# Optimization experiments

Hardware: AMD Instinct MI355X
Metric: run time of the kernel (lower is better)

Reference implementation:

```python
import jax, jax.numpy as jnp
import numpy as np

D_IN, E, K = 128, 256, 16
LN_EPS = 1e-5


def _layernorm(h, g, b):
    mu = jnp.mean(h, axis=-1, keepdims=True)
    var = jnp.mean(jnp.square(h - mu), axis=-1, keepdims=True)
    return (h - mu) * jax.lax.rsqrt(var + LN_EPS) * g + b


def _gelu(h):
    return jax.nn.gelu(h, approximate=False)  # torch F.gelu default = exact erf


def setup_inputs() -> dict:
    key = jax.random.key(0)
    ks = jax.random.split(key, 8)
    B, N = 8, 2048
    def lin(k, fan_in, fan_out):
        bound = 1.0 / np.sqrt(fan_in)
        return jax.random.uniform(k, (fan_in, fan_out), jnp.float32, -bound, bound)
    return {
        "x": jax.random.normal(ks[0], (B, N, D_IN), jnp.float32),
        "coordinates": jax.random.normal(ks[1], (B, N, 3), jnp.float32),
        "W1": lin(ks[2], 2 * D_IN, E), "b1": jnp.zeros((E,), jnp.float32),
        "g1": jnp.ones((E,), jnp.float32), "be1": jnp.zeros((E,), jnp.float32),
        "W2": lin(ks[3], E, E), "b2": jnp.zeros((E,), jnp.float32),
        "g2": jnp.ones((E,), jnp.float32), "be2": jnp.zeros((E,), jnp.float32),
        "W3": lin(ks[4], E, E), "b3": jnp.zeros((E,), jnp.float32),
        "g3": jnp.ones((E,), jnp.float32), "be3": jnp.zeros((E,), jnp.float32),
        "Ws": lin(ks[5], D_IN, E), "bs": jnp.zeros((E,), jnp.float32),
    }


def reference(x, coordinates, W1, b1, g1, be1, W2, b2, g2, be2, W3, b3, g3, be3, Ws, bs):
    B, N, D = x.shape
    # --- dynamic kNN graph: squared euclidean distances (sqrt is monotone, skip it) ---
    sq = jnp.sum(coordinates * coordinates, axis=-1)                 # [B,N]
    d2 = sq[:, :, None] + sq[:, None, :] - 2.0 * jnp.einsum(
        'bnc,bmc->bnm', coordinates, coordinates)                    # [B,N,N]
    d2 = jnp.maximum(d2, 0.0)
    _, idx = jax.lax.top_k(-d2, K)                                   # [B,N,K] nearest (incl. self)
    # --- gather neighbor features: neighbors[b,n,j] = x[b, idx[b,n,j]] ---
    neighbors = jax.vmap(lambda xb, ib: xb[ib])(x, idx)              # [B,N,K,D]
    central = jnp.broadcast_to(x[:, :, None, :], (B, N, K, D))       # [B,N,K,D]
    edge = jnp.concatenate([central, neighbors - central], axis=-1)  # [B,N,K,2D]
    # --- edge MLP: (Linear -> LN -> GELU) x3 ---
    h = _gelu(_layernorm(edge @ W1 + b1, g1, be1))
    h = _gelu(_layernorm(h @ W2 + b2, g2, be2))
    h = _gelu(_layernorm(h @ W3 + b3, g3, be3))                      # [B,N,K,E]
    # --- max aggregate over neighbors + shortcut ---
    agg = jnp.max(h, axis=2)                                         # [B,N,E]
    return _gelu(agg + x @ Ws + bs)
```

## Files before the change

### kernel.cpp

```cpp
#include <hip/hip_runtime.h>
#include <hip/hip_bf16.h>
#include <math.h>

#define B_ 8
#define N_ 2048
#define D_ 128
#define E_ 256
#define K_ 16
#define LN_EPS 1e-5f

typedef short bf16x8 __attribute__((ext_vector_type(8)));
typedef float f32x4 __attribute__((ext_vector_type(4)));
typedef float f32x2 __attribute__((ext_vector_type(2)));

__device__ __forceinline__ float sq3_ref(float x, float y, float z) {
#pragma clang fp contract(off)
    float s = x * x + y * y;
    s = s + z * z;
    return s;
}
__device__ __forceinline__ float d2_ref(float qx, float qy, float qz, float sqq,
                                        float mx, float my, float mz, float sqm) {
#pragma clang fp contract(off)
    float dot = mx * qx + my * qy;
    dot = dot + mz * qz;
    float t1 = sqq + sqm;
    float t2 = 2.0f * dot;
    float d2 = t1 - t2;
    return d2 > 0.0f ? d2 : 0.0f;
}

__device__ __forceinline__ unsigned pack2(float a, float b) {
    union { __hip_bfloat162 h2; unsigned u; } cv;
    cv.h2 = __float22bfloat162_rn(float2{a, b});
    return cv.u;
}

__device__ __forceinline__ f32x2 gelu2(f32x2 v) {
    const f32x2 w = v * v;
    f32x2 inner = w * 0.044715f;
    inner.x += 1.0f; inner.y += 1.0f;
    const f32x2 ue = (v * -2.3022083f) * inner;
    f32x2 t;
    t.x = __builtin_amdgcn_exp2f(ue.x);
    t.y = __builtin_amdgcn_exp2f(ue.y);
    f32x2 den = t;
    den.x += 1.0f; den.y += 1.0f;
    f32x2 r;
    r.x = __builtin_amdgcn_rcpf(den.x);
    r.y = __builtin_amdgcn_rcpf(den.y);
    return v * r;
}

__device__ __forceinline__ float dpp_rowmax16(float v) {
    int x = __float_as_int(v);
    v = fmaxf(v, __int_as_float(__builtin_amdgcn_mov_dpp(x, 0xB1, 0xF, 0xF, true)));
    x = __float_as_int(v);
    v = fmaxf(v, __int_as_float(__builtin_amdgcn_mov_dpp(x, 0x4E, 0xF, 0xF, true)));
    x = __float_as_int(v);
    v = fmaxf(v, __int_as_float(__builtin_amdgcn_mov_dpp(x, 0x141, 0xF, 0xF, true)));
    x = __float_as_int(v);
    v = fmaxf(v, __int_as_float(__builtin_amdgcn_mov_dpp(x, 0x140, 0xF, 0xF, true)));
    return v;
}

__global__ __launch_bounds__(512) void prep_kernel(
    const float* __restrict__ coords, const float* __restrict__ x,
    const float* __restrict__ W1, const float* __restrict__ W2,
    const float* __restrict__ W3, const float* __restrict__ Ws,
    const float* __restrict__ bs,
    int* __restrict__ knn_out, short* __restrict__ WF, float* __restrict__ out)
{
    __shared__ float smem[4 * N_ + 8];
    const int bid = blockIdx.x;
    const int tid = threadIdx.x;

    if (bid < 2048) {
        float (*lc)[N_] = (float(*)[N_])smem;
        float* lsq = smem + 3 * N_;
        int* cnt = (int*)(smem + 4 * N_);
        const int wave = tid >> 6;
        const int lane = tid & 63;
        const int p = bid * 8 + wave;
        const int b = p >> 11;
        const int n0 = p & (N_ - 1);
        const float* cb = coords + (size_t)b * N_ * 3;
        for (int i = tid; i < N_ * 3; i += 512) {
            int n = i / 3, c = i - 3 * n;
            lc[c][n] = cb[i];
        }
        __syncthreads();
        for (int n = tid; n < N_; n += 512) lsq[n] = sq3_ref(lc[0][n], lc[1][n], lc[2][n]);
        __syncthreads();

        const float qx = lc[0][n0], qy = lc[1][n0], qz = lc[2][n0], sqq = lsq[n0];
        unsigned key[32];
#pragma unroll
        for (int j = 0; j < 32; ++j) {
            const int m = j * 64 + lane;
            key[j] = __float_as_uint(d2_ref(qx, qy, qz, sqq, lc[0][m], lc[1][m], lc[2][m], lsq[m]));
        }

        unsigned prefix = 0;
        int rem = K_, setc = N_, bshift = 0;
        bool bounded = false;
        for (int bit = 31; bit >= 0; --bit) {
            const unsigned want = prefix << 1;
            int c = 0;
#pragma unroll
            for (int j = 0; j < 32; ++j) c += ((key[j] >> bit) == want) ? 1 : 0;
            for (int off = 1; off < 64; off <<= 1) c += __shfl_xor(c, off, 64);
            if (rem <= c) { prefix = want; setc = c; }
            else          { prefix = want | 1u; rem -= c; setc -= c; }
            bshift = bit;
            if (setc == rem) { bounded = true; break; }
        }

        if (lane == 0) cnt[wave] = 0;
        int* op = knn_out + (size_t)p * K_;
        const unsigned long long BE = bounded ? (((unsigned long long)prefix + 1ull) << bshift)
                                              : (unsigned long long)prefix;
#pragma unroll
        for (int j = 0; j < 32; ++j) {
            if ((unsigned long long)key[j] < BE) {
                int s = atomicAdd(&cnt[wave], 1);
                op[s] = j * 64 + lane;
            }
        }
        if (!bounded) {
            const unsigned V = prefix;
#pragma unroll
            for (int j = 0; j < 32; ++j) {
                if (rem > 0) {
                    unsigned long long mask = __ballot(key[j] == V);
                    int below = __popcll(mask & ((1ull << lane) - 1ull));
                    if (key[j] == V && below < rem) {
                        int s = atomicAdd(&cnt[wave], 1);
                        op[s] = j * 64 + lane;
                    }
                    rem -= __popcll(mask);
                }
            }
        }
    } else if (bid < 2096) {
        const int unit = (bid - 2048) * 8 + (tid >> 6);
        const int lane = tid & 63;
        const int g = lane >> 4, e = lane & 15;
        const int L = unit >> 7;
        const int t = unit & 127;
        const int kt = t >> 4, mt = t & 15;
        const float* W = (L == 0) ? W1 : (L == 1) ? W2 : W3;
        const int f = 16 * mt + e;
        unsigned v[4];
#pragma unroll
        for (int i2 = 0; i2 < 4; ++i2) {
            const int k = 32 * kt + 8 * g + 2 * i2;
            v[i2] = pack2(W[(size_t)k * E_ + f], W[(size_t)(k + 1) * E_ + f]);
        }
        uint4 u; u.x = v[0]; u.y = v[1]; u.z = v[2]; u.w = v[3];
        *reinterpret_cast<uint4*>(WF + ((size_t)unit * 64 + lane) * 8) = u;
    } else {
        const int wave = tid >> 6;
        const int lane = tid & 63;
        const int e = lane & 15;
        const int g = lane >> 4;
        const int p0 = ((bid - 2096) * 8 + wave) * 16;
        const float* xr = x + (size_t)(p0 + e) * D_;

        f32x4 acc[16];
        const f32x4 z4 = {0.f, 0.f, 0.f, 0.f};
#pragma unroll
        for (int mt = 0; mt < 16; ++mt) acc[mt] = z4;

#pragma unroll
        for (int kt = 0; kt < 4; ++kt) {
            const float4 xa = *(const float4*)(xr + kt * 32 + g * 8);
            const float4 xb = *(const float4*)(xr + kt * 32 + g * 8 + 4);
            union { unsigned u[4]; bf16x8 v; } bx;
            bx.u[0] = pack2(xa.x, xa.y); bx.u[1] = pack2(xa.z, xa.w);
            bx.u[2] = pack2(xb.x, xb.y); bx.u[3] = pack2(xb.z, xb.w);
            const float* Wsrc = Ws + (size_t)(32 * kt + 8 * g) * E_ + e;
#pragma unroll
            for (int mt = 0; mt < 16; ++mt) {
                const float* wp = Wsrc + 16 * mt;
                float w[8];
#pragma unroll
                for (int i = 0; i < 8; ++i) w[i] = wp[(size_t)i * E_];
                union { unsigned u[4]; bf16x8 v; } a;
                a.u[0] = pack2(w[0], w[1]); a.u[1] = pack2(w[2], w[3]);
                a.u[2] = pack2(w[4], w[5]); a.u[3] = pack2(w[6], w[7]);
                acc[mt] = __builtin_amdgcn_mfma_f32_16x16x32_bf16(a.v, bx.v, acc[mt], 0, 0, 0);
            }
        }
#pragma unroll
        for (int mt = 0; mt < 16; ++mt) {
            const float4 bsv = *(const float4*)(bs + 16 * mt + 4 * g);
            float4 o;
            o.x = acc[mt][0] + bsv.x; o.y = acc[mt][1] + bsv.y;
            o.z = acc[mt][2] + bsv.z; o.w = acc[mt][3] + bsv.w;
            *(float4*)(out + (size_t)(p0 + e) * E_ + 16 * mt + 4 * g) = o;
        }
    }
}

#define WCHUNKS 24

__device__ __forceinline__ void stage_chunk(const short* __restrict__ WF,
                                            short* __restrict__ dst,
                                            int c, int wave, int lane) {
    const short* src = WF + ((size_t)(c << 4) << 9);
#pragma unroll
    for (int i = 0; i < 4; ++i) {
        const int slot = (i << 8) + (wave << 6);
        const short* gp = src + ((size_t)(slot + lane) << 3);
        short* lp = dst + ((size_t)slot << 3);
        __builtin_amdgcn_global_load_lds(
            (const __attribute__((address_space(1))) void*)gp,
            (__attribute__((address_space(3))) void*)lp, 16, 0, 0);
    }
}

__global__ __launch_bounds__(256, 3) void edgeconv_mfma(
    const float* __restrict__ x, const int* __restrict__ knn,
    const short* __restrict__ WF,
    const float* __restrict__ b1, const float* __restrict__ g1, const float* __restrict__ be1,
    const float* __restrict__ b2, const float* __restrict__ g2, const float* __restrict__ be2,
    const float* __restrict__ b3, const float* __restrict__ g3, const float* __restrict__ be3,
    float* __restrict__ out)
{
    __shared__ short Hl[2][2][4096];
    __shared__ short Wbuf[8192];
    __shared__ float4 Xch[2][2][16];
    __shared__ float Pl[768];
    const int tid  = threadIdx.x;
    const int wave = tid >> 6;
    const int lane = tid & 63;
    const int wq = wave & 1;
    const int pr = wave >> 1;
    const int e = lane & 15;
    const int g = lane >> 4;
    const int p = blockIdx.x * 4 + wave;
    const int b = p >> 11;
    const int n = p & (N_ - 1);
    const unsigned swz = (unsigned)((e & 7) << 4);
    char* Hown = (char*)&Hl[pr][wq][0];
    char* Hp0  = (char*)&Hl[pr][0][0];
    char* Hp1  = (char*)&Hl[pr][1][0];

    {
        const float4* xr = (const float4*)(x + ((size_t)b * N_ + n) * D_);
        const int nb = knn[(size_t)p * K_ + e];
        const float4* nr = (const float4*)(x + ((size_t)b * N_ + nb) * D_);
#pragma unroll
        for (int c2 = 0; c2 < 8; ++c2) {
            const float4 cv = xr[8 * g + c2];
            const float4 nv = nr[8 * g + c2];
            const int base = (e << 9) + (g << 6) + (c2 << 3);
            *(uint2*)(Hown + (base ^ swz)) = make_uint2(pack2(cv.x, cv.y), pack2(cv.z, cv.w));
            *(uint2*)(Hown + ((base + 256) ^ swz)) =
                make_uint2(pack2(nv.x - cv.x, nv.y - cv.y), pack2(nv.z - cv.z, nv.w - cv.w));
        }
    }

    f32x4 acc0[8], acc1[8];
    const f32x4 z4 = {0.f, 0.f, 0.f, 0.f};

    for (int L = 0; L < 3; ++L) {
        const float* bL  = (L == 0) ? b1  : (L == 1) ? b2  : b3;
        const float* gL  = (L == 0) ? g1  : (L == 1) ? g2  : g3;
        const float* beL = (L == 0) ? be1 : (L == 1) ? be2 : be3;
#pragma unroll
        for (int mtl = 0; mtl < 8; ++mtl) { acc0[mtl] = z4; acc1[mtl] = z4; }

        for (int kt = 0; kt < 8; ++kt) {
            const int c = L * 8 + kt;
            __syncthreads();
            const int offB = (int)((unsigned)((e << 9) + (kt << 6) + (g << 4)) ^ swz);
            const bf16x8 Bc0 = *(const bf16x8*)(Hp0 + offB);
            const bf16x8 Bc1 = *(const bf16x8*)(Hp1 + offB);
            stage_chunk(WF, Wbuf, c, wave, lane);
            asm volatile("s_waitcnt vmcnt(0)" ::: "memory");
            __syncthreads();
            if (kt == 0) {
                Pl[tid]       = bL[tid];
                Pl[256 + tid] = gL[tid];
                Pl[512 + tid] = beL[tid];
            }
            __builtin_amdgcn_s_setprio(1);
#pragma unroll
            for (int mtl = 0; mtl < 8; ++mtl) {
                const bf16x8 a = *(const bf16x8*)(Wbuf + ((((wq << 3) + mtl) << 6) + lane) * 8);
                acc0[mtl] = __builtin_amdgcn_mfma_f32_16x16x32_bf16(a, Bc0, acc0[mtl], 0, 0, 0);
                acc1[mtl] = __builtin_amdgcn_mfma_f32_16x16x32_bf16(a, Bc1, acc1[mtl], 0, 0, 0);
            }
            __builtin_amdgcn_s_setprio(0);
        }

        f32x2 s2_0 = {0.f, 0.f}, q2_0 = {0.f, 0.f};
        f32x2 s2_1 = {0.f, 0.f}, q2_1 = {0.f, 0.f};
#pragma unroll
        for (int mtl = 0; mtl < 8; ++mtl) {
            const int mtg = (wq << 3) + mtl;
            const float4 bv = *(const float4*)(Pl + mtg * 16 + (g << 2));
            const f32x2 blo = {bv.x, bv.y}, bhi = {bv.z, bv.w};
            f32x2 a0lo = {acc0[mtl][0], acc0[mtl][1]};
            f32x2 a0hi = {acc0[mtl][2], acc0[mtl][3]};
            f32x2 a1lo = {acc1[mtl][0], acc1[mtl][1]};
            f32x2 a1hi = {acc1[mtl][2], acc1[mtl][3]};
            a0lo = a0lo + blo; a0hi = a0hi + bhi;
            a1lo = a1lo + blo; a1hi = a1hi + bhi;
            s2_0 = s2_0 + a0lo; s2_0 = s2_0 + a0hi;
            q2_0 = q2_0 + a0lo * a0lo; q2_0 = q2_0 + a0hi * a0hi;
            s2_1 = s2_1 + a1lo; s2_1 = s2_1 + a1hi;
            q2_1 = q2_1 + a1lo * a1lo; q2_1 = q2_1 + a1hi * a1hi;
            acc0[mtl][0] = a0lo.x; acc0[mtl][1] = a0lo.y;
            acc0[mtl][2] = a0hi.x; acc0[mtl][3] = a0hi.y;
            acc1[mtl][0] = a1lo.x; acc1[mtl][1] = a1lo.y;
            acc1[mtl][2] = a1hi.x; acc1[mtl][3] = a1hi.y;
        }
        float s0 = s2_0.x + s2_0.y, q0 = q2_0.x + q2_0.y;
        float s1 = s2_1.x + s2_1.y, q1 = q2_1.x + q2_1.y;
        s0 += __shfl_xor(s0, 16, 64); s0 += __shfl_xor(s0, 32, 64);
        q0 += __shfl_xor(q0, 16, 64); q0 += __shfl_xor(q0, 32, 64);
        s1 += __shfl_xor(s1, 16, 64); s1 += __shfl_xor(s1, 32, 64);
        q1 += __shfl_xor(q1, 16, 64); q1 += __shfl_xor(q1, 32, 64);
        if (lane < 16) Xch[pr][wq][e] = make_float4(s0, q0, s1, q1);
        __syncthreads();
        const float4 oX = Xch[pr][wq ^ 1][e];
        const float mu0 = (s0 + oX.x) * (1.0f / 256.0f);
        const float var0 = fmaf(-mu0, mu0, (q0 + oX.y) * (1.0f / 256.0f));
        const float rstd0 = rsqrtf(var0 + LN_EPS);
        const float mu1 = (s1 + oX.z) * (1.0f / 256.0f);
        const float var1 = fmaf(-mu1, mu1, (q1 + oX.w) * (1.0f / 256.0f));
        const float rstd1 = rsqrtf(var1 + LN_EPS);

#pragma unroll
        for (int mtl = 0; mtl < 8; ++mtl) {
            const int mtg = (wq << 3) + mtl;
            const float4 gv  = *(const float4*)(Pl + 256 + mtg * 16 + (g << 2));
            const float4 bev = *(const float4*)(Pl + 512 + mtg * 16 + (g << 2));
            const f32x2 glo = {gv.x, gv.y}, ghi = {gv.z, gv.w};
            const f32x2 belo = {bev.x, bev.y}, behi = {bev.z, bev.w};
            const f32x2 A0lo = glo * rstd0, A0hi = ghi * rstd0;
            const f32x2 C0lo = A0lo * (-mu0) + belo, C0hi = A0hi * (-mu0) + behi;
            const f32x2 v0lo = {acc0[mtl][0], acc0[mtl][1]};
            const f32x2 v0hi = {acc0[mtl][2], acc0[mtl][3]};
            const f32x2 r0lo = gelu2(v0lo * A0lo + C0lo);
            const f32x2 r0hi = gelu2(v0hi * A0hi + C0hi);
            const f32x2 A1lo = glo * rstd1, A1hi = ghi * rstd1;
            const f32x2 C1lo = A1lo * (-mu1) + belo, C1hi = A1hi * (-mu1) + behi;
            const f32x2 v1lo = {acc1[mtl][0], acc1[mtl][1]};
            const f32x2 v1hi = {acc1[mtl][2], acc1[mtl][3]};
            const f32x2 r1lo = gelu2(v1lo * A1lo + C1lo);
            const f32x2 r1hi = gelu2(v1hi * A1hi + C1hi);
            if (L < 2) {
                const int wb = (int)((unsigned)((e << 9) + (mtg << 5) + (g << 3)) ^ swz);
                *(uint2*)(Hp0 + wb) = make_uint2(pack2(r0lo.x, r0lo.y), pack2(r0hi.x, r0hi.y));
                *(uint2*)(Hp1 + wb) = make_uint2(pack2(r1lo.x, r1lo.y), pack2(r1hi.x, r1hi.y));
            } else {
                acc0[mtl][0] = r0lo.x; acc0[mtl][1] = r0lo.y;
                acc0[mtl][2] = r0hi.x; acc0[mtl][3] = r0hi.y;
                acc1[mtl][0] = r1lo.x; acc1[mtl][1] = r1lo.y;
                acc1[mtl][2] = r1hi.x; acc1[mtl][3] = r1hi.y;
            }
        }
    }

#pragma unroll
    for (int mtl = 0; mtl < 8; ++mtl) {
#pragma unroll
        for (int i = 0; i < 4; ++i) {
            acc0[mtl][i] = dpp_rowmax16(acc0[mtl][i]);
            acc1[mtl][i] = dpp_rowmax16(acc1[mtl][i]);
        }
    }
    float* Sb0 = (float*)Hp0;
    float* Sb1 = (float*)Hp1;
#pragma unroll
    for (int mtl = 0; mtl < 8; ++mtl) {
        if (e == mtl) {
            const int fo = (((wq << 3) + mtl) << 4) + (g << 2);
            *(float4*)(Sb0 + fo) = *(const float4*)&acc0[mtl];
            *(float4*)(Sb1 + fo) = *(const float4*)&acc1[mtl];
        }
    }
    __syncthreads();

    const int f0 = 16 * e + (g << 2);
    const float* SbO = wq ? Sb1 : Sb0;
    const float4 agg = *(const float4*)(SbO + f0);
    float* op = out + (size_t)p * E_ + f0;
    const float4 ssc = *(const float4*)op;
    f32x2 elo = {agg.x + ssc.x, agg.y + ssc.y};
    f32x2 ehi = {agg.z + ssc.z, agg.w + ssc.w};
    const f32x2 olo = gelu2(elo);
    const f32x2 ohi = gelu2(ehi);
    float4 o;
    o.x = olo.x; o.y = olo.y; o.z = ohi.x; o.w = ohi.y;
    *(float4*)op = o;
}

extern "C" void kernel_launch(void* const* d_in, const int* in_sizes, int n_in,
                              void* d_out, int out_size, void* d_ws, size_t ws_size,
                              hipStream_t stream) {
    const float* x      = (const float*)d_in[0];
    const float* coords = (const float*)d_in[1];
    const float* W1  = (const float*)d_in[2];
    const float* b1  = (const float*)d_in[3];
    const float* g1  = (const float*)d_in[4];
    const float* be1 = (const float*)d_in[5];
    const float* W2  = (const float*)d_in[6];
    const float* b2  = (const float*)d_in[7];
    const float* g2  = (const float*)d_in[8];
    const float* be2 = (const float*)d_in[9];
    const float* W3  = (const float*)d_in[10];
    const float* b3  = (const float*)d_in[11];
    const float* g3  = (const float*)d_in[12];
    const float* be3 = (const float*)d_in[13];
    const float* Ws  = (const float*)d_in[14];
    const float* bs  = (const float*)d_in[15];
    float* out = (float*)d_out;

    int*   knn = (int*)d_ws;
    short* WF  = (short*)((char*)d_ws + (1 << 20));

    prep_kernel<<<2048 + 48 + 128, 512, 0, stream>>>(
        coords, x, W1, W2, W3, Ws, bs, knn, WF, out);
    edgeconv_mfma<<<(B_ * N_) / 4, 256, 0, stream>>>(
        x, knn, WF, b1, g1, be1, b2, g2, be2, b3, g3, be3, out);
}
```

Before: 296.1 us.

## Read MFMA weight fragments directly from global, drop LDS staging and per-k-tile barriers

New measurement: 302.0 us. No clear change (+2.0%).

```diff
diff --git a/kernel.cpp b/kernel.cpp
--- a/kernel.cpp
+++ b/kernel.cpp
@@ -203,23 +203,6 @@
     }
 }
 
-#define WCHUNKS 24
-
-__device__ __forceinline__ void stage_chunk(const short* __restrict__ WF,
-                                            short* __restrict__ dst,
-                                            int c, int wave, int lane) {
-    const short* src = WF + ((size_t)(c << 4) << 9);
-#pragma unroll
-    for (int i = 0; i < 4; ++i) {
-        const int slot = (i << 8) + (wave << 6);
-        const short* gp = src + ((size_t)(slot + lane) << 3);
-        short* lp = dst + ((size_t)slot << 3);
-        __builtin_amdgcn_global_load_lds(
-            (const __attribute__((address_space(1))) void*)gp,
-            (__attribute__((address_space(3))) void*)lp, 16, 0, 0);
-    }
-}
-
 __global__ __launch_bounds__(256, 3) void edgeconv_mfma(
     const float* __restrict__ x, const int* __restrict__ knn,
     const short* __restrict__ WF,
@@ -229,9 +212,8 @@
     float* __restrict__ out)
 {
     __shared__ short Hl[2][2][4096];
-    __shared__ short Wbuf[8192];
     __shared__ float4 Xch[2][2][16];
-    __shared__ float Pl[768];
+    __shared__ float Pl[9 * 256];
     const int tid  = threadIdx.x;
     const int wave = tid >> 6;
     const int lane = tid & 63;
@@ -248,6 +230,12 @@
     char* Hp1  = (char*)&Hl[pr][1][0];
 
     {
+        const float* srcs[9] = {b1, g1, be1, b2, g2, be2, b3, g3, be3};
+#pragma unroll
+        for (int a = 0; a < 9; ++a) Pl[a * 256 + tid] = srcs[a][tid];
+    }
+
+    {
         const float4* xr = (const float4*)(x + ((size_t)b * N_ + n) * D_);
         const int nb = knn[(size_t)p * K_ + e];
         const float4* nr = (const float4*)(x + ((size_t)b * N_ + nb) * D_);
@@ -261,35 +249,27 @@
                 make_uint2(pack2(nv.x - cv.x, nv.y - cv.y), pack2(nv.z - cv.z, nv.w - cv.w));
         }
     }
+    __syncthreads();
 
     f32x4 acc0[8], acc1[8];
     const f32x4 z4 = {0.f, 0.f, 0.f, 0.f};
 
     for (int L = 0; L < 3; ++L) {
-        const float* bL  = (L == 0) ? b1  : (L == 1) ? b2  : b3;
-        const float* gL  = (L == 0) ? g1  : (L == 1) ? g2  : g3;
-        const float* beL = (L == 0) ? be1 : (L == 1) ? be2 : be3;
+        const float* PlL = &Pl[L * 768];
 #pragma unroll
         for (int mtl = 0; mtl < 8; ++mtl) { acc0[mtl] = z4; acc1[mtl] = z4; }
 
+        const short* AL = WF + (((size_t)(L * 128 + wq * 8)) << 9);
+
         for (int kt = 0; kt < 8; ++kt) {
-            const int c = L * 8 + kt;
-            __syncthreads();
             const int offB = (int)((unsigned)((e << 9) + (kt << 6) + (g << 4)) ^ swz);
             const bf16x8 Bc0 = *(const bf16x8*)(Hp0 + offB);
             const bf16x8 Bc1 = *(const bf16x8*)(Hp1 + offB);
-            stage_chunk(WF, Wbuf, c, wave, lane);
-            asm volatile("s_waitcnt vmcnt(0)" ::: "memory");
-            __syncthreads();
-            if (kt == 0) {
-                Pl[tid]       = bL[tid];
-                Pl[256 + tid] = gL[tid];
-                Pl[512 + tid] = beL[tid];
-            }
+            const short* Ak = AL + ((size_t)kt << 13);
             __builtin_amdgcn_s_setprio(1);
 #pragma unroll
             for (int mtl = 0; mtl < 8; ++mtl) {
-                const bf16x8 a = *(const bf16x8*)(Wbuf + ((((wq << 3) + mtl) << 6) + lane) * 8);
+                const bf16x8 a = *(const bf16x8*)(Ak + (mtl << 9) + (lane << 3));
                 acc0[mtl] = __builtin_amdgcn_mfma_f32_16x16x32_bf16(a, Bc0, acc0[mtl], 0, 0, 0);
                 acc1[mtl] = __builtin_amdgcn_mfma_f32_16x16x32_bf16(a, Bc1, acc1[mtl], 0, 0, 0);
             }
@@ -301,7 +281,7 @@
 #pragma unroll
         for (int mtl = 0; mtl < 8; ++mtl) {
             const int mtg = (wq << 3) + mtl;
-            const float4 bv = *(const float4*)(Pl + mtg * 16 + (g << 2));
+            const float4 bv = *(const float4*)(PlL + mtg * 16 + (g << 2));
             const f32x2 blo = {bv.x, bv.y}, bhi = {bv.z, bv.w};
             f32x2 a0lo = {acc0[mtl][0], acc0[mtl][1]};
             f32x2 a0hi = {acc0[mtl][2], acc0[mtl][3]};
@@ -337,8 +317,8 @@
 #pragma unroll
         for (int mtl = 0; mtl < 8; ++mtl) {
             const int mtg = (wq << 3) + mtl;
-            const float4 gv  = *(const float4*)(Pl + 256 + mtg * 16 + (g << 2));
-            const float4 bev = *(const float4*)(Pl + 512 + mtg * 16 + (g << 2));
+            const float4 gv  = *(const float4*)(PlL + 256 + mtg * 16 + (g << 2));
+            const float4 bev = *(const float4*)(PlL + 512 + mtg * 16 + (g << 2));
             const f32x2 glo = {gv.x, gv.y}, ghi = {gv.z, gv.w};
             const f32x2 belo = {bev.x, bev.y}, behi = {bev.z, bev.w};
             const f32x2 A0lo = glo * rstd0, A0hi = ghi * rstd0;
@@ -364,6 +344,7 @@
                 acc1[mtl][2] = r1hi.x; acc1[mtl][3] = r1hi.y;
             }
         }
+        if (L < 2) __syncthreads();
     }
 
 #pragma unroll
```
